# Optimization experiments

Hardware: AMD Instinct MI355X
Metric: run time of the kernel (lower is better)

## Reference

```python
import jax, jax.numpy as jnp
import numpy as np

B, T, E, H = 8, 2048, 512, 16
D = E // H  # 32 embeddings per head
LN_EPS = 1e-3  # keras LayerNormalization default epsilon
DECAY = 1.2


def setup_inputs() -> dict:
    key = jax.random.key(0)
    k0, k1, k2 = jax.random.split(key, 3)
    x = jax.random.normal(k0, (B, T, E), dtype=jnp.float32)
    W = jax.random.normal(k1, (E, E), dtype=jnp.float32) * (1.0 / np.sqrt(E))
    b = jnp.zeros((E,), dtype=jnp.float32)
    concept_map = jax.random.normal(k2, (H, D, D, D), dtype=jnp.float32) * 0.02
    gamma = jnp.ones((E,), dtype=jnp.float32)
    beta = jnp.zeros((E,), dtype=jnp.float32)
    return {"x": x, "W": W, "b": b, "concept_map": concept_map,
            "gamma": gamma, "beta": beta}


def reference(x, W, b, concept_map, gamma, beta):
    Bn, Tn, En = x.shape
    Hn = concept_map.shape[0]
    Dn = En // Hn
    # Dense projection, split into heads: (B,T,H,D)
    h = (jnp.einsum('bte,ef->btf', x, W) + b).reshape(Bn, Tn, Hn, Dn)
    # Decayed cumulative sum of preceding tokens: S_0 = 0, S_t = (S_{t-1} + h_{t-1}) / 1.2
    def step(s, h_t):
        return (s + h_t) / DECAY, s
    _, S = jax.lax.scan(step, jnp.zeros((Bn, Hn, Dn), h.dtype),
                        jnp.swapaxes(h, 0, 1))  # S: (T,B,H,D)
    S = jnp.swapaxes(S, 0, 1)  # (B,T,H,D)
    # Fused bilinear contraction: sum_{i,j} h[...,i] * S[...,j] * C[h,k,i,j]
    # (equivalent to outer-product * concept_map then reduce_sum over last two dims)
    y = jnp.einsum('bthi,bthj,hkij->bthk', h, S, concept_map) + h
    y = y.reshape(Bn, Tn, En)
    # LayerNormalization over last axis (keras default eps=1e-3)
    mu = jnp.mean(y, axis=-1, keepdims=True)
    var = jnp.var(y, axis=-1, keepdims=True)
    y = (y - mu) * jax.lax.rsqrt(var + LN_EPS) * gamma + beta
    # Dropout: identity at inference
    return y
```

## Files before the change

### kernel.cpp

```cpp
#include <hip/hip_runtime.h>
#include <hip/hip_bf16.h>

#define Bn 8
#define Tn 2048
#define En 512
#define Hn 16
#define Dn 32
#define NC 32
#define CL 64
#define NT (Bn*Tn)
#define INV_DECAY (1.0f/1.2f)

typedef __attribute__((ext_vector_type(8))) short  bf16x8;
typedef __attribute__((ext_vector_type(4))) float  f32x4;
typedef __attribute__((ext_vector_type(8))) unsigned short u16x8;

__device__ __forceinline__ unsigned short f2b(float f) {
    __hip_bfloat16 h = __float2bfloat16(f);
    return *reinterpret_cast<unsigned short*>(&h);
}
__device__ __forceinline__ float b2f(unsigned short u) {
    union { unsigned int i; float f; } c; c.i = ((unsigned int)u) << 16; return c.f;
}

__device__ __forceinline__ size_t hm(int hd, int tok, int ch) {
    return (size_t)hd * ((size_t)NT * Dn) + (size_t)tok * Dn + ch;
}

__global__ __launch_bounds__(256) void prep_k(const float* __restrict__ C,
                                              unsigned short* __restrict__ Cl,
                                              const float* __restrict__ W,
                                              unsigned short* __restrict__ Wt) {
    __shared__ float tile[32][33];
    if (blockIdx.x < 256) {
        const int g = blockIdx.x * 256 + threadIdx.x;
        const int hd = g >> 12, rem = g & 4095;
        const int i = rem >> 7, half = (rem >> 6) & 1, lane = rem & 63;
        const int tloc = lane & 15, kgrp = lane >> 4;
        const int k = half * 16 + tloc;
        const float* src = C + (size_t)hd * 32768 + (size_t)k * 1024 + i * 32 + kgrp * 8;
        float4 a = reinterpret_cast<const float4*>(src)[0];
        float4 b = reinterpret_cast<const float4*>(src)[1];
        u16x8 st;
        st[0]=f2b(a.x); st[1]=f2b(a.y); st[2]=f2b(a.z); st[3]=f2b(a.w);
        st[4]=f2b(b.x); st[5]=f2b(b.y); st[6]=f2b(b.z); st[7]=f2b(b.w);
        *reinterpret_cast<u16x8*>(Cl + (size_t)g * 8) = st;
    } else {
        const int bid = blockIdx.x - 256;
        const int kb = (bid & 15) * 32, nb = (bid >> 4) * 32;
        const int tx = threadIdx.x & 31, ty = threadIdx.x >> 5;
        #pragma unroll
        for (int j = 0; j < 4; j++)
            tile[ty + 8 * j][tx] = W[(size_t)(kb + ty + 8 * j) * En + nb + tx];
        __syncthreads();
        #pragma unroll
        for (int j = 0; j < 4; j++)
            Wt[(size_t)(nb + ty + 8 * j) * En + kb + tx] = f2b(tile[tx][ty + 8 * j]);
    }
}

__global__ __launch_bounds__(256) void gemm_mfma_k(const float* __restrict__ x,
                                                   const unsigned short* __restrict__ Wt,
                                                   const float* __restrict__ bias,
                                                   unsigned short* __restrict__ h) {
    __shared__ unsigned short As[128][40];
    __shared__ unsigned short Bs[64][40];
    const int m0 = blockIdx.x * 128, n0 = blockIdx.y * 64;
    const int tid = threadIdx.x;
    const int wid = tid >> 6, lane = tid & 63;
    const int tloc = lane & 15, kgrp = lane >> 4;
    const int wr = wid >> 1, wc = wid & 1;

    const int ar = tid >> 1, ah = (tid & 1) * 16;
    const int brr = tid >> 2, bq = (tid & 3) * 8;

    f32x4 acc[4][2] = {};

    for (int k0 = 0; k0 < En; k0 += 32) {
        const float* xp = &x[(size_t)(m0 + ar) * En + k0 + ah];
        float4 a0 = reinterpret_cast<const float4*>(xp)[0];
        float4 a1 = reinterpret_cast<const float4*>(xp)[1];
        float4 a2 = reinterpret_cast<const float4*>(xp)[2];
        float4 a3 = reinterpret_cast<const float4*>(xp)[3];
        u16x8 bv = *reinterpret_cast<const u16x8*>(&Wt[(size_t)(n0 + brr) * En + k0 + bq]);
        __syncthreads();
        u16x8 w0, w1;
        w0[0]=f2b(a0.x); w0[1]=f2b(a0.y); w0[2]=f2b(a0.z); w0[3]=f2b(a0.w);
        w0[4]=f2b(a1.x); w0[5]=f2b(a1.y); w0[6]=f2b(a1.z); w0[7]=f2b(a1.w);
        w1[0]=f2b(a2.x); w1[1]=f2b(a2.y); w1[2]=f2b(a2.z); w1[3]=f2b(a2.w);
        w1[4]=f2b(a3.x); w1[5]=f2b(a3.y); w1[6]=f2b(a3.z); w1[7]=f2b(a3.w);
        *reinterpret_cast<u16x8*>(&As[ar][ah])     = w0;
        *reinterpret_cast<u16x8*>(&As[ar][ah + 8]) = w1;
        *reinterpret_cast<u16x8*>(&Bs[brr][bq])    = bv;
        __syncthreads();

        bf16x8 afr[4], bfr[2];
        #pragma unroll
        for (int m = 0; m < 4; m++)
            afr[m] = *reinterpret_cast<const bf16x8*>(&As[wr * 64 + m * 16 + tloc][kgrp * 8]);
        #pragma unroll
        for (int n = 0; n < 2; n++)
            bfr[n] = *reinterpret_cast<const bf16x8*>(&Bs[wc * 32 + n * 16 + tloc][kgrp * 8]);
        #pragma unroll
        for (int m = 0; m < 4; m++)
            #pragma unroll
            for (int n = 0; n < 2; n++)
                acc[m][n] = __builtin_amdgcn_mfma_f32_16x16x32_bf16(afr[m], bfr[n], acc[m][n], 0, 0, 0);
    }

    #pragma unroll
    for (int n = 0; n < 2; n++) {
        const int col = n0 + wc * 32 + n * 16 + tloc;
        const float bcol = bias[col];
        const int hd = col >> 5, ch = col & 31;
        #pragma unroll
        for (int m = 0; m < 4; m++)
            #pragma unroll
            for (int r = 0; r < 4; r++) {
                const int row = m0 + wr * 64 + m * 16 + kgrp * 4 + r;
                h[hm(hd, row, ch)] = f2b(acc[m][n][r] + bcol);
            }
    }
}

__global__ __launch_bounds__(512) void scan_local_k(const unsigned short* __restrict__ h,
                                                    float* __restrict__ locals) {
    const int c = blockIdx.x, b = blockIdx.y;
    const int e = threadIdx.x;
    const int hd = e >> 5, ch = e & 31;
    const unsigned short* hp = h + hm(hd, b * Tn + c * CL, ch);
    float s = 0.f;
    for (int t = 0; t < CL; t++) s = (s + b2f(hp[(size_t)t * Dn])) * INV_DECAY;
    locals[(size_t)(b * NC + c) * En + e] = s;
}

__global__ __launch_bounds__(512) void scan_prefix_k(const float* __restrict__ locals,
                                                     float* __restrict__ Acar) {
    const int b = blockIdx.x;
    const int e = threadIdx.x;
    float invRL = 1.f;
    #pragma unroll
    for (int i = 0; i < CL; i++) invRL *= INV_DECAY;
    float A = 0.f;
    for (int c = 0; c < NC; c++) {
        Acar[(size_t)(b * NC + c) * En + e] = A;
        A = A * invRL + locals[(size_t)(b * NC + c) * En + e];
    }
}

__global__ __launch_bounds__(512) void scan_emit_k(const unsigned short* __restrict__ h,
                                                   const float* __restrict__ Acar,
                                                   unsigned short* __restrict__ Sg) {
    const int c = blockIdx.x, b = blockIdx.y;
    const int e = threadIdx.x;
    const int hd = e >> 5, ch = e & 31;
    float s = Acar[(size_t)(b * NC + c) * En + e];
    const size_t base = hm(hd, b * Tn + c * CL, ch);
    for (int t = 0; t < CL; t++) {
        Sg[base + (size_t)t * Dn] = f2b(s);
        s = (s + b2f(h[base + (size_t)t * Dn])) * INV_DECAY;
    }
}

__global__ __launch_bounds__(256, 3) void bilinear8_k(const unsigned short* __restrict__ hg,
                                                      unsigned short* __restrict__ Sio,
                                                      const unsigned short* __restrict__ Cl) {
    __shared__ float ys[4][64][36];

    const int hd = blockIdx.y;
    const int tid = threadIdx.x;
    const int wid = tid >> 6, lane = tid & 63;
    const int tloc = lane & 15, kgrp = lane >> 4;
    const int j0 = kgrp * 8;
    const int tokens0 = blockIdx.x * 64;

    bf16x8 afr[8][2];
    {
        const unsigned short* cb = Cl + (size_t)hd * 32768;
        #pragma unroll
        for (int s = 0; s < 8; s++) {
            const int i = wid * 8 + s;
            #pragma unroll
            for (int mt = 0; mt < 2; mt++)
                afr[s][mt] = *reinterpret_cast<const bf16x8*>(
                    cb + ((size_t)((i * 2 + mt) * 64 + lane) * 8));
        }
    }

    u16x8 hreg[4];
    float sf[4][8];
    #pragma unroll
    for (int nt = 0; nt < 4; nt++) {
        const int trow = tokens0 + nt * 16 + tloc;
        hreg[nt] = *reinterpret_cast<const u16x8*>(hg + hm(hd, trow, wid * 8));
        u16x8 sv = *reinterpret_cast<const u16x8*>(Sio + hm(hd, trow, j0));
        #pragma unroll
        for (int e = 0; e < 8; e++) sf[nt][e] = b2f(sv[e]);
    }

    f32x4 acc[2][4] = {};
    #pragma unroll
    for (int s = 0; s < 8; s++) {
        #pragma unroll
        for (int nt = 0; nt < 4; nt++) {
            const float hsc = b2f(hreg[nt][s]);
            bf16x8 bfrag;
            #pragma unroll
            for (int e = 0; e < 8; e++) bfrag[e] = (short)f2b(hsc * sf[nt][e]);
            acc[0][nt] = __builtin_amdgcn_mfma_f32_16x16x32_bf16(afr[s][0], bfrag, acc[0][nt], 0, 0, 0);
            acc[1][nt] = __builtin_amdgcn_mfma_f32_16x16x32_bf16(afr[s][1], bfrag, acc[1][nt], 0, 0, 0);
        }
    }

    #pragma unroll
    for (int mt = 0; mt < 2; mt++)
        #pragma unroll
        for (int nt = 0; nt < 4; nt++)
            *reinterpret_cast<f32x4*>(&ys[wid][nt * 16 + tloc][mt * 16 + kgrp * 4]) = acc[mt][nt];
    __syncthreads();

    {
        const int token = tid >> 2, q = tid & 3;
        float y[8];
        #pragma unroll
        for (int e = 0; e < 8; e++) y[e] = 0.f;
        #pragma unroll
        for (int w = 0; w < 4; w++) {
            const float* src = &ys[w][token][q * 8];
            #pragma unroll
            for (int e = 0; e < 8; e++) y[e] += src[e];
        }
        const unsigned short* hrow = hg + hm(hd, tokens0 + token, q * 8);
        u16x8 hres = *reinterpret_cast<const u16x8*>(hrow);
        u16x8 st;
        #pragma unroll
        for (int e = 0; e < 8; e++) st[e] = f2b(y[e] + b2f(hres[e]));
        *reinterpret_cast<u16x8*>(Sio + hm(hd, tokens0 + token, q * 8)) = st;
    }
}

__global__ __launch_bounds__(256) void ln_k(const unsigned short* __restrict__ y,
                                            const float* __restrict__ gamma,
                                            const float* __restrict__ beta,
                                            float* __restrict__ out) {
    const int row = blockIdx.x * 4 + (threadIdx.x >> 6);
    const int lane = threadIdx.x & 63;
    u16x8 v = *reinterpret_cast<const u16x8*>(y + hm(lane >> 2, row, (lane & 3) * 8));
    float f[8];
    float s = 0.f, s2 = 0.f;
    #pragma unroll
    for (int e = 0; e < 8; e++) {
        f[e] = b2f(v[e]);
        s += f[e]; s2 += f[e] * f[e];
    }
    #pragma unroll
    for (int off = 1; off < 64; off <<= 1) {
        s  += __shfl_xor(s, off);
        s2 += __shfl_xor(s2, off);
    }
    const float mu = s * (1.f / En);
    const float var = s2 * (1.f / En) - mu * mu;
    const float rs = rsqrtf(var + 1e-3f);
    const int cbase = lane * 8;
    float4 g0 = reinterpret_cast<const float4*>(&gamma[cbase])[0];
    float4 g1 = reinterpret_cast<const float4*>(&gamma[cbase])[1];
    float4 b0 = reinterpret_cast<const float4*>(&beta[cbase])[0];
    float4 b1 = reinterpret_cast<const float4*>(&beta[cbase])[1];
    float4 o0, o1;
    o0.x = (f[0] - mu) * rs * g0.x + b0.x; o0.y = (f[1] - mu) * rs * g0.y + b0.y;
    o0.z = (f[2] - mu) * rs * g0.z + b0.z; o0.w = (f[3] - mu) * rs * g0.w + b0.w;
    o1.x = (f[4] - mu) * rs * g1.x + b1.x; o1.y = (f[5] - mu) * rs * g1.y + b1.y;
    o1.z = (f[6] - mu) * rs * g1.z + b1.z; o1.w = (f[7] - mu) * rs * g1.w + b1.w;
    float* op = out + (size_t)row * En;
    reinterpret_cast<float4*>(op)[lane * 2]     = o0;
    reinterpret_cast<float4*>(op)[lane * 2 + 1] = o1;
}

extern "C" void kernel_launch(void* const* d_in, const int* in_sizes, int n_in,
                              void* d_out, int out_size, void* d_ws, size_t ws_size,
                              hipStream_t stream) {
    const float* x     = (const float*)d_in[0];
    const float* W     = (const float*)d_in[1];
    const float* bias  = (const float*)d_in[2];
    const float* C     = (const float*)d_in[3];
    const float* gamma = (const float*)d_in[4];
    const float* beta  = (const float*)d_in[5];
    float* out = (float*)d_out;

    unsigned short* hb  = (unsigned short*)d_ws;
    unsigned short* Sg  = hb + (size_t)Hn * NT * Dn;
    unsigned short* Cl  = Sg + (size_t)Hn * NT * Dn;
    unsigned short* Wt  = Cl + (size_t)Hn * Dn * Dn * Dn;
    float* locals = (float*)(Wt + (size_t)En * En);
    float* Acar   = locals + (size_t)Bn * NC * En;

    prep_k<<<512, 256, 0, stream>>>(C, Cl, W, Wt);
    gemm_mfma_k<<<dim3(NT / 128, En / 64), 256, 0, stream>>>(x, Wt, bias, hb);
    scan_local_k<<<dim3(NC, Bn), 512, 0, stream>>>(hb, locals);
    scan_prefix_k<<<Bn, 512, 0, stream>>>(locals, Acar);
    scan_emit_k<<<dim3(NC, Bn), 512, 0, stream>>>(hb, Acar, Sg);
    bilinear8_k<<<dim3(NT / 64, Hn), 256, 0, stream>>>(hb, Sg, Cl);
    ln_k<<<NT / 4, 256, 0, stream>>>(Sg, gamma, beta, out);
}
```

Baseline: 83.55 us.

## Fuse chunk-local scan into GEMM epilogue and scan emit into bilinear kernel

The GEMM epilogue now computes each 64-token chunk's decayed local sum directly from the bf16 outputs, weighting each row by a precomputed decay power and reducing across lanes with shuffles. This removes the separate scan_local kernel. The bilinear kernel stages h for its 64-token tile in shared memory and regenerates S from the chunk carry with a 32-thread sequential scan, which removes scan_emit and the global S round-trip. The cost is a serial 64-step loop run by only 32 threads inside the bilinear kernel, plus extra LDS, which may reduce occupancy.

Result: no change. 82.29 us (-1.5%).

```diff
diff --git a/kernel.cpp b/kernel.cpp
--- a/kernel.cpp
+++ b/kernel.cpp
@@ -21,6 +21,12 @@
 }
 __device__ __forceinline__ float b2f(unsigned short u) {
     union { unsigned int i; float f; } c; c.i = ((unsigned int)u) << 16; return c.f;
+}
+
+__host__ __device__ constexpr float wpow(int e) {
+    float r = 1.f;
+    for (int i = 0; i < e; i++) r *= (1.0f / 1.2f);
+    return r;
 }
 
 __device__ __forceinline__ size_t hm(int hd, int tok, int ch) {
@@ -62,7 +68,8 @@
 __global__ __launch_bounds__(256) void gemm_mfma_k(const float* __restrict__ x,
                                                    const unsigned short* __restrict__ Wt,
                                                    const float* __restrict__ bias,
-                                                   unsigned short* __restrict__ h) {
+                                                   unsigned short* __restrict__ h,
+                                                   float* __restrict__ locals) {
     __shared__ unsigned short As[128][40];
     __shared__ unsigned short Bs[64][40];
     const int m0 = blockIdx.x * 128, n0 = blockIdx.y * 64;
@@ -108,30 +115,28 @@
                 acc[m][n] = __builtin_amdgcn_mfma_f32_16x16x32_bf16(afr[m], bfr[n], acc[m][n], 0, 0, 0);
     }
 
+    const float kmul = (kgrp & 1 ? 2.0736f : 1.f) * (kgrp & 2 ? 4.29981696f : 1.f);
+    const int cg = blockIdx.x * 2 + wr;
+
     #pragma unroll
     for (int n = 0; n < 2; n++) {
         const int col = n0 + wc * 32 + n * 16 + tloc;
         const float bcol = bias[col];
         const int hd = col >> 5, ch = col & 31;
+        float part = 0.f;
         #pragma unroll
         for (int m = 0; m < 4; m++)
             #pragma unroll
             for (int r = 0; r < 4; r++) {
                 const int row = m0 + wr * 64 + m * 16 + kgrp * 4 + r;
-                h[hm(hd, row, ch)] = f2b(acc[m][n][r] + bcol);
+                const unsigned short hb16 = f2b(acc[m][n][r] + bcol);
+                h[hm(hd, row, ch)] = hb16;
+                part += b2f(hb16) * (wpow(64 - m * 16 - r) * kmul);
             }
-    }
-}
-
-__global__ __launch_bounds__(512) void scan_local_k(const unsigned short* __restrict__ h,
-                                                    float* __restrict__ locals) {
-    const int c = blockIdx.x, b = blockIdx.y;
-    const int e = threadIdx.x;
-    const int hd = e >> 5, ch = e & 31;
-    const unsigned short* hp = h + hm(hd, b * Tn + c * CL, ch);
-    float s = 0.f;
-    for (int t = 0; t < CL; t++) s = (s + b2f(hp[(size_t)t * Dn])) * INV_DECAY;
-    locals[(size_t)(b * NC + c) * En + e] = s;
+        part += __shfl_xor(part, 16);
+        part += __shfl_xor(part, 32);
+        if (kgrp == 0) locals[(size_t)cg * En + col] = part;
+    }
 }
 
 __global__ __launch_bounds__(512) void scan_prefix_k(const float* __restrict__ locals,
@@ -148,31 +153,21 @@
     }
 }
 
-__global__ __launch_bounds__(512) void scan_emit_k(const unsigned short* __restrict__ h,
-                                                   const float* __restrict__ Acar,
-                                                   unsigned short* __restrict__ Sg) {
-    const int c = blockIdx.x, b = blockIdx.y;
-    const int e = threadIdx.x;
-    const int hd = e >> 5, ch = e & 31;
-    float s = Acar[(size_t)(b * NC + c) * En + e];
-    const size_t base = hm(hd, b * Tn + c * CL, ch);
-    for (int t = 0; t < CL; t++) {
-        Sg[base + (size_t)t * Dn] = f2b(s);
-        s = (s + b2f(h[base + (size_t)t * Dn])) * INV_DECAY;
-    }
-}
-
-__global__ __launch_bounds__(256, 3) void bilinear8_k(const unsigned short* __restrict__ hg,
-                                                      unsigned short* __restrict__ Sio,
+__global__ __launch_bounds__(256, 3) void bilinear9_k(const unsigned short* __restrict__ hg,
+                                                      const float* __restrict__ Acar,
+                                                      unsigned short* __restrict__ yb,
                                                       const unsigned short* __restrict__ Cl) {
+    __shared__ unsigned short hs[64][40];
+    __shared__ unsigned short Ss[64][40];
     __shared__ float ys[4][64][36];
 
     const int hd = blockIdx.y;
+    const int cg = blockIdx.x;
+    const int tokens0 = cg * 64;
     const int tid = threadIdx.x;
     const int wid = tid >> 6, lane = tid & 63;
     const int tloc = lane & 15, kgrp = lane >> 4;
     const int j0 = kgrp * 8;
-    const int tokens0 = blockIdx.x * 64;
 
     bf16x8 afr[8][2];
     {
@@ -187,13 +182,29 @@
         }
     }
 
+    {
+        const int tok = tid >> 2, c8 = (tid & 3) * 8;
+        u16x8 v = *reinterpret_cast<const u16x8*>(hg + hm(hd, tokens0 + tok, c8));
+        *reinterpret_cast<u16x8*>(&hs[tok][c8]) = v;
+    }
+    __syncthreads();
+
+    if (tid < Dn) {
+        float s = Acar[(size_t)cg * En + hd * Dn + tid];
+        for (int t = 0; t < 64; t++) {
+            Ss[t][tid] = f2b(s);
+            s = (s + b2f(hs[t][tid])) * INV_DECAY;
+        }
+    }
+    __syncthreads();
+
     u16x8 hreg[4];
     float sf[4][8];
     #pragma unroll
     for (int nt = 0; nt < 4; nt++) {
-        const int trow = tokens0 + nt * 16 + tloc;
-        hreg[nt] = *reinterpret_cast<const u16x8*>(hg + hm(hd, trow, wid * 8));
-        u16x8 sv = *reinterpret_cast<const u16x8*>(Sio + hm(hd, trow, j0));
+        const int trow = nt * 16 + tloc;
+        hreg[nt] = *reinterpret_cast<const u16x8*>(&hs[trow][wid * 8]);
+        u16x8 sv = *reinterpret_cast<const u16x8*>(&Ss[trow][j0]);
         #pragma unroll
         for (int e = 0; e < 8; e++) sf[nt][e] = b2f(sv[e]);
     }
@@ -230,12 +241,11 @@
             #pragma unroll
             for (int e = 0; e < 8; e++) y[e] += src[e];
         }
-        const unsigned short* hrow = hg + hm(hd, tokens0 + token, q * 8);
-        u16x8 hres = *reinterpret_cast<const u16x8*>(hrow);
+        u16x8 hres = *reinterpret_cast<const u16x8*>(&hs[token][q * 8]);
         u16x8 st;
         #pragma unroll
         for (int e = 0; e < 8; e++) st[e] = f2b(y[e] + b2f(hres[e]));
-        *reinterpret_cast<u16x8*>(Sio + hm(hd, tokens0 + token, q * 8)) = st;
+        *reinterpret_cast<u16x8*>(yb + hm(hd, tokens0 + token, q * 8)) = st;
     }
 }
 
@@ -288,17 +298,15 @@
     float* out = (float*)d_out;
 
     unsigned short* hb  = (unsigned short*)d_ws;
-    unsigned short* Sg  = hb + (size_t)Hn * NT * Dn;
-    unsigned short* Cl  = Sg + (size_t)Hn * NT * Dn;
+    unsigned short* yb  = hb + (size_t)Hn * NT * Dn;
+    unsigned short* Cl  = yb + (size_t)Hn * NT * Dn;
     unsigned short* Wt  = Cl + (size_t)Hn * Dn * Dn * Dn;
     float* locals = (float*)(Wt + (size_t)En * En);
     float* Acar   = locals + (size_t)Bn * NC * En;
 
     prep_k<<<512, 256, 0, stream>>>(C, Cl, W, Wt);
-    gemm_mfma_k<<<dim3(NT / 128, En / 64), 256, 0, stream>>>(x, Wt, bias, hb);
-    scan_local_k<<<dim3(NC, Bn), 512, 0, stream>>>(hb, locals);
+    gemm_mfma_k<<<dim3(NT / 128, En / 64), 256, 0, stream>>>(x, Wt, bias, hb, locals);
     scan_prefix_k<<<Bn, 512, 0, stream>>>(locals, Acar);
-    scan_emit_k<<<dim3(NC, Bn), 512, 0, stream>>>(hb, Acar, Sg);
-    bilinear8_k<<<dim3(NT / 64, Hn), 256, 0, stream>>>(hb, Sg, Cl);
-    ln_k<<<NT / 4, 256, 0, stream>>>(Sg, gamma, beta, out);
-}
+    bilinear9_k<<<dim3(NT / CL, Hn), 256, 0, stream>>>(hb, Acar, yb, Cl);
+    ln_k<<<NT / 4, 256, 0, stream>>>(yb, gamma, beta, out);
+}
```

## Fuse chunk-local decayed scan into GEMM epilogue and drop scan_local kernel

Applied to the files above, without the earlier changes.

The GEMM epilogue now computes each 64-token chunk's decayed local sum directly from its bf16-rounded outputs, weighting them by precomputed powers of 1/1.2 and reducing across lanes with shuffles. This removes the separate scan_local kernel, along with its launch and its re-read of h. The bilinear kernel's occupancy hint goes from 3 to 4 blocks and its residual reduction is vectorised. Summing with weights instead of a sequential recurrence changes the rounding slightly, and the higher occupancy target may force register spilling.

Measured after the change: 81.91 us. About the same (-2.0%).

```diff
diff --git a/kernel.cpp b/kernel.cpp
--- a/kernel.cpp
+++ b/kernel.cpp
@@ -21,6 +21,12 @@
 }
 __device__ __forceinline__ float b2f(unsigned short u) {
     union { unsigned int i; float f; } c; c.i = ((unsigned int)u) << 16; return c.f;
+}
+
+__host__ __device__ constexpr float wpow(int e) {
+    float r = 1.f;
+    for (int i = 0; i < e; i++) r *= (1.0f / 1.2f);
+    return r;
 }
 
 __device__ __forceinline__ size_t hm(int hd, int tok, int ch) {
@@ -62,7 +68,8 @@
 __global__ __launch_bounds__(256) void gemm_mfma_k(const float* __restrict__ x,
                                                    const unsigned short* __restrict__ Wt,
                                                    const float* __restrict__ bias,
-                                                   unsigned short* __restrict__ h) {
+                                                   unsigned short* __restrict__ h,
+                                                   float* __restrict__ locals) {
     __shared__ unsigned short As[128][40];
     __shared__ unsigned short Bs[64][40];
     const int m0 = blockIdx.x * 128, n0 = blockIdx.y * 64;
@@ -108,30 +115,28 @@
                 acc[m][n] = __builtin_amdgcn_mfma_f32_16x16x32_bf16(afr[m], bfr[n], acc[m][n], 0, 0, 0);
     }
 
+    const float kmul = (kgrp & 1 ? 2.0736f : 1.f) * (kgrp & 2 ? 4.29981696f : 1.f);
+    const int cg = blockIdx.x * 2 + wr;
+
     #pragma unroll
     for (int n = 0; n < 2; n++) {
         const int col = n0 + wc * 32 + n * 16 + tloc;
         const float bcol = bias[col];
         const int hd = col >> 5, ch = col & 31;
+        float part = 0.f;
         #pragma unroll
         for (int m = 0; m < 4; m++)
             #pragma unroll
             for (int r = 0; r < 4; r++) {
                 const int row = m0 + wr * 64 + m * 16 + kgrp * 4 + r;
-                h[hm(hd, row, ch)] = f2b(acc[m][n][r] + bcol);
+                const unsigned short hb16 = f2b(acc[m][n][r] + bcol);
+                h[hm(hd, row, ch)] = hb16;
+                part += b2f(hb16) * (wpow(64 - m * 16 - r) * kmul);
             }
-    }
-}
-
-__global__ __launch_bounds__(512) void scan_local_k(const unsigned short* __restrict__ h,
-                                                    float* __restrict__ locals) {
-    const int c = blockIdx.x, b = blockIdx.y;
-    const int e = threadIdx.x;
-    const int hd = e >> 5, ch = e & 31;
-    const unsigned short* hp = h + hm(hd, b * Tn + c * CL, ch);
-    float s = 0.f;
-    for (int t = 0; t < CL; t++) s = (s + b2f(hp[(size_t)t * Dn])) * INV_DECAY;
-    locals[(size_t)(b * NC + c) * En + e] = s;
+        part += __shfl_xor(part, 16);
+        part += __shfl_xor(part, 32);
+        if (kgrp == 0) locals[(size_t)cg * En + col] = part;
+    }
 }
 
 __global__ __launch_bounds__(512) void scan_prefix_k(const float* __restrict__ locals,
@@ -162,9 +167,10 @@
     }
 }
 
-__global__ __launch_bounds__(256, 3) void bilinear8_k(const unsigned short* __restrict__ hg,
-                                                      unsigned short* __restrict__ Sio,
-                                                      const unsigned short* __restrict__ Cl) {
+__global__ __launch_bounds__(256, 4) void bilinear12_k(const unsigned short* __restrict__ hg,
+                                                       const unsigned short* __restrict__ Sg,
+                                                       unsigned short* __restrict__ yb,
+                                                       const unsigned short* __restrict__ Cl) {
     __shared__ float ys[4][64][36];
 
     const int hd = blockIdx.y;
@@ -193,7 +199,7 @@
     for (int nt = 0; nt < 4; nt++) {
         const int trow = tokens0 + nt * 16 + tloc;
         hreg[nt] = *reinterpret_cast<const u16x8*>(hg + hm(hd, trow, wid * 8));
-        u16x8 sv = *reinterpret_cast<const u16x8*>(Sio + hm(hd, trow, j0));
+        u16x8 sv = *reinterpret_cast<const u16x8*>(Sg + hm(hd, trow, j0));
         #pragma unroll
         for (int e = 0; e < 8; e++) sf[nt][e] = b2f(sv[e]);
     }
@@ -221,21 +227,21 @@
 
     {
         const int token = tid >> 2, q = tid & 3;
-        float y[8];
-        #pragma unroll
-        for (int e = 0; e < 8; e++) y[e] = 0.f;
+        f32x4 y0 = {0.f,0.f,0.f,0.f}, y1 = {0.f,0.f,0.f,0.f};
         #pragma unroll
         for (int w = 0; w < 4; w++) {
-            const float* src = &ys[w][token][q * 8];
-            #pragma unroll
-            for (int e = 0; e < 8; e++) y[e] += src[e];
+            const f32x4* src = reinterpret_cast<const f32x4*>(&ys[w][token][q * 8]);
+            y0 += src[0];
+            y1 += src[1];
         }
-        const unsigned short* hrow = hg + hm(hd, tokens0 + token, q * 8);
-        u16x8 hres = *reinterpret_cast<const u16x8*>(hrow);
+        u16x8 hres = *reinterpret_cast<const u16x8*>(hg + hm(hd, tokens0 + token, q * 8));
         u16x8 st;
         #pragma unroll
-        for (int e = 0; e < 8; e++) st[e] = f2b(y[e] + b2f(hres[e]));
-        *reinterpret_cast<u16x8*>(Sio + hm(hd, tokens0 + token, q * 8)) = st;
+        for (int e = 0; e < 4; e++) {
+            st[e]     = f2b(y0[e] + b2f(hres[e]));
+            st[4 + e] = f2b(y1[e] + b2f(hres[4 + e]));
+        }
+        *reinterpret_cast<u16x8*>(yb + hm(hd, tokens0 + token, q * 8)) = st;
     }
 }
 
@@ -295,10 +301,9 @@
     float* Acar   = locals + (size_t)Bn * NC * En;
 
     prep_k<<<512, 256, 0, stream>>>(C, Cl, W, Wt);
-    gemm_mfma_k<<<dim3(NT / 128, En / 64), 256, 0, stream>>>(x, Wt, bias, hb);
-    scan_local_k<<<dim3(NC, Bn), 512, 0, stream>>>(hb, locals);
+    gemm_mfma_k<<<dim3(NT / 128, En / 64), 256, 0, stream>>>(x, Wt, bias, hb, locals);
     scan_prefix_k<<<Bn, 512, 0, stream>>>(locals, Acar);
     scan_emit_k<<<dim3(NC, Bn), 512, 0, stream>>>(hb, Acar, Sg);
-    bilinear8_k<<<dim3(NT / 64, Hn), 256, 0, stream>>>(hb, Sg, Cl);
+    bilinear12_k<<<dim3(NT / CL, Hn), 256, 0, stream>>>(hb, Sg, Sg , Cl);
     ln_k<<<NT / 4, 256, 0, stream>>>(Sg, gamma, beta, out);
 }
```
